# Optimization experiments

Measured on AMD Instinct MI355X. Metric: run time of the kernel, lower is better.

The kernel has to match this reference:

```python
import jax, jax.numpy as jnp
import numpy as np

B, HR, WR, C, HEADS, WS = 32, 64, 64, 128, 4, 8
HD = C // HEADS            # head dim = 32
N = WS * WS                # tokens per window = 64
NB = (2 * WS - 1) ** 2     # relative-bias table rows = 225
EPS = 1e-5


def _relative_bias_index():
    # Static int index, identical to SwinMSA._get_relative_bias_index
    coords = np.stack(np.meshgrid(np.arange(WS), np.arange(WS), indexing='ij'))  # (2, ws, ws)
    flat = coords.reshape(2, -1)                      # (2, n)
    rel = flat[:, :, None] - flat[:, None, :]         # (2, n, n)
    rel = rel.transpose(1, 2, 0).copy()               # (n, n, 2)
    rel[:, :, 0] += WS - 1
    rel[:, :, 1] += WS - 1
    rel[:, :, 0] *= 2 * WS - 1
    return rel.sum(-1)                                # (n, n) int

_REL_IDX = _relative_bias_index()


def _ln(x, g, b):
    m = jnp.mean(x, axis=-1, keepdims=True)
    v = jnp.mean(jnp.square(x - m), axis=-1, keepdims=True)
    return (x - m) * jax.lax.rsqrt(v + EPS) * g + b


def setup_inputs() -> dict:
    key = jax.random.key(0)
    ks = jax.random.split(key, 16)
    s = 0.02
    return {
        'x': jax.random.normal(ks[0], (B, HR * WR, C), jnp.float32),
        'qkv_w': jax.random.normal(ks[1], (C, 3 * C), jnp.float32) * s,
        'qkv_b': jnp.zeros((3 * C,), jnp.float32),
        'proj_w': jax.random.normal(ks[2], (C, C), jnp.float32) * s,
        'proj_b': jnp.zeros((C,), jnp.float32),
        'rel_bias_table': jax.random.normal(ks[3], (NB, HEADS), jnp.float32) * s,
        'ln1_g': jnp.ones((C,), jnp.float32),
        'ln1_b': jnp.zeros((C,), jnp.float32),
        'ln2_g': jnp.ones((C,), jnp.float32),
        'ln2_b': jnp.zeros((C,), jnp.float32),
        'mlp_w1': jax.random.normal(ks[4], (C, 4 * C), jnp.float32) * s,
        'mlp_b1': jnp.zeros((4 * C,), jnp.float32),
        'mlp_w2': jax.random.normal(ks[5], (4 * C, C), jnp.float32) * s,
        'mlp_b2': jnp.zeros((C,), jnp.float32),
    }


def reference(x, qkv_w, qkv_b, proj_w, proj_b, rel_bias_table,
              ln1_g, ln1_b, ln2_g, ln2_b, mlp_w1, mlp_b1, mlp_w2, mlp_b2):
    b = x.shape[0]
    hb, wb = HR // WS, WR // WS
    img = x.reshape(b, HR, WR, C)
    n1 = _ln(img, ln1_g, ln1_b)
    # window_partition: '(wy h) (wx w)' split puts window coord OUTER (strided windows),
    # faithful to the source rearrange.
    part = n1.reshape(b, WS, hb, WS, wb, C).transpose(0, 2, 4, 1, 3, 5)
    part = part.reshape(b * hb * wb, N, C)            # (Bw, n, c)
    qkv = part @ qkv_w + qkv_b                        # (Bw, n, 3c)
    # rearrange 'b n (h d c) -> d b n h c': channel factors as (head, 3, head_dim)
    qkv = qkv.reshape(-1, N, HEADS, 3, HD)
    q, k, v = qkv[..., 0, :], qkv[..., 1, :], qkv[..., 2, :]   # (Bw, n, h, hd)
    energy = jnp.einsum('bqhe,bkhe->bqhk', q, k) * (HD ** -0.5)
    bias = rel_bias_table[_REL_IDX.reshape(-1)].reshape(N, N, HEADS)
    bias = bias.transpose(2, 0, 1)                    # (h, n, n)
    energy = energy + bias.transpose(1, 0, 2)[None]   # broadcast as (q, h, k)
    attn = jax.nn.softmax(energy, axis=-1)
    out = jnp.einsum('bihv,bvhd->bihd', attn, v).reshape(-1, N, C)
    out = out @ proj_w + proj_b                       # (Bw, n, c)
    # window_reverse (inverse of the strided partition)
    rev = out.reshape(b, hb, wb, WS, WS, C).transpose(0, 3, 1, 4, 2, 5)
    rev = rev.reshape(b, HR * WR, C)
    msa = x + rev
    h2 = _ln(msa, ln2_g, ln2_b)
    mlp = jax.nn.gelu(h2 @ mlp_w1 + mlp_b1, approximate=False) @ mlp_w2 + mlp_b2
    return msa + mlp
```

## Files before the change

### kernel.cpp

```cpp
#include <hip/hip_runtime.h>
#include <hip/hip_bf16.h>

typedef __attribute__((ext_vector_type(4))) float f32x4;
typedef __attribute__((ext_vector_type(8))) short bf16x8;
typedef __attribute__((ext_vector_type(4))) short bf16x4;
typedef unsigned short u16;

__device__ __forceinline__ short fbf(float f){
  __hip_bfloat16 h = __float2bfloat16(f);
  return *reinterpret_cast<short*>(&h);
}
__device__ __forceinline__ float bf2f(short s){
  return __uint_as_float(((unsigned)(unsigned short)s) << 16);
}

#define LOG2E 1.4426950408889634f

__global__ void repack_kernel(const float* __restrict__ qkv_w, const float* __restrict__ proj_w,
                              const float* __restrict__ w1, const float* __restrict__ w2,
                              const float* __restrict__ tbl,
                              u16* __restrict__ rq, u16* __restrict__ rp,
                              u16* __restrict__ r1, u16* __restrict__ r2,
                              float* __restrict__ be){
  const int i = blockIdx.x * 256 + threadIdx.x;
  const int j = i & 7, lane = (i >> 3) & 63, f = i >> 9;
  const int kr = (lane >> 4) * 8 + j;
  const int c16 = lane & 15;
  if (i < 49152){ int nt = f % 24, kk = f / 24; rq[i] = (u16)fbf(qkv_w[(kk*32 + kr)*384 + nt*16 + c16]); }
  if (i < 16384){ int nt = f & 7,  kk = f >> 3; rp[i] = (u16)fbf(proj_w[(kk*32 + kr)*128 + nt*16 + c16]); }
  if (i < 65536){ int nt = f & 31, kk = f >> 5; r1[i] = (u16)fbf(w1[(kk*32 + kr)*512 + nt*16 + c16]); }
  if (i < 65536){ int nt = f & 7,  kk = f >> 3; r2[i] = (u16)fbf(w2[(kk*32 + kr)*128 + nt*16 + c16]); }
  if (i < 16384){
    int rg = i & 3, ln = (i >> 2) & 63, g = i >> 8;
    int nt = g & 3, mt = (g >> 2) & 3, h = g >> 4;
    int row = mt*16 + (ln >> 4)*4 + rg;
    int col = nt*16 + (ln & 15);
    int rel = ((col >> 3) - (row >> 3) + 7) * 15 + ((col & 7) - (row & 7) + 7);
    be[i] = tbl[rel*4 + h] * LOG2E;
  }
}

__global__ __launch_bounds__(256, 3)
void block_kernel(const float* __restrict__ x,
                  const float* __restrict__ qkv_b, const float* __restrict__ proj_b,
                  const float* __restrict__ ln1_g, const float* __restrict__ ln1_b,
                  const float* __restrict__ ln2_g, const float* __restrict__ ln2_b,
                  const u16* __restrict__ rep_qkv, const u16* __restrict__ rep_proj,
                  const u16* __restrict__ rep_w1, const u16* __restrict__ rep_w2,
                  const float* __restrict__ mlp_b1, const float* __restrict__ mlp_b2,
                  const float* __restrict__ bias_exp,
                  float* __restrict__ out){
  __shared__ __align__(16) u16 smem[24576];
  u16* sLN = smem;
  u16* sQ  = smem;
  u16* sK  = smem + 8192;
  u16* sV  = smem + 16384;
  u16* sP  = smem;
  u16* sO  = smem;
  u16* stg = smem + 8192;
  u16* sH  = smem + 16384;
  u16* sG  = smem;

  const int tid = threadIdx.x, lane = tid & 63, wid = tid >> 6;
  const int wdw = blockIdx.x;
  const int bb = wdw >> 6, ihb = (wdw >> 3) & 7, iwb = wdw & 7;
  const float* xb = x + (size_t)bb * 4096 * 128;
  float* ob = out + (size_t)bb * 4096 * 128;
  const f32x4 z4 = {0.f, 0.f, 0.f, 0.f};
  const int rb = tid >> 4, cb = tid & 15, c0g = cb * 8;
  const int r15 = lane & 15, kg = lane >> 4;

  {
    float g8[8], b8[8];
    *(f32x4*)&g8[0] = *(const f32x4*)(ln1_g + c0g);
    *(f32x4*)&g8[4] = *(const f32x4*)(ln1_g + c0g + 4);
    *(f32x4*)&b8[0] = *(const f32x4*)(ln1_b + c0g);
    *(f32x4*)&b8[4] = *(const f32x4*)(ln1_b + c0g + 4);
    #pragma unroll
    for (int it = 0; it < 4; ++it){
      const int r = it * 16 + rb;
      const int pix = ((r >> 3) * 8 + ihb) * 64 + (r & 7) * 8 + iwb;
      float fl[8];
      *(f32x4*)&fl[0] = *(const f32x4*)(xb + (size_t)pix * 128 + c0g);
      *(f32x4*)&fl[4] = *(const f32x4*)(xb + (size_t)pix * 128 + c0g + 4);
      float s = 0.f, sq = 0.f;
      #pragma unroll
      for (int j = 0; j < 8; ++j){ s += fl[j]; sq += fl[j]*fl[j]; }
      #pragma unroll
      for (int m = 1; m < 16; m <<= 1){ s += __shfl_xor(s, m); sq += __shfl_xor(sq, m); }
      const float mean = s * (1.f/128.f);
      const float rs = __builtin_amdgcn_rsqf(sq * (1.f/128.f) - mean*mean + 1e-5f);
      bf16x8 o;
      #pragma unroll
      for (int j = 0; j < 8; ++j) o[j] = fbf((fl[j]-mean)*rs*g8[j] + b8[j]);
      *(bf16x8*)&sLN[r*128 + (c0g ^ ((r & 7) << 3))] = o;
    }
  }
  __syncthreads();

  {
    f32x4 aqk[4][4];
    f32x4 av[4][2];
    #pragma unroll
    for (int ct = 0; ct < 4; ++ct){
      const f32x4 bq = *(const f32x4*)(qkv_b + wid*96 + ct*16 + kg*4);
      #pragma unroll
      for (int tt = 0; tt < 4; ++tt) aqk[ct][tt] = bq;
    }
    #pragma unroll
    for (int nt = 0; nt < 2; ++nt){
      const float bv = qkv_b[wid*96 + 64 + nt*16 + r15];
      const f32x4 bv4 = {bv, bv, bv, bv};
      #pragma unroll
      for (int mt = 0; mt < 4; ++mt) av[mt][nt] = bv4;
    }
    #pragma unroll
    for (int kk = 0; kk < 4; ++kk){
      bf16x8 L[4], aW[4], bWv[2];
      const int c0 = kk*32 + kg*8;
      #pragma unroll
      for (int t = 0; t < 4; ++t){
        const int row = t*16 + r15;
        L[t] = *(const bf16x8*)&sLN[row*128 + (c0 ^ ((row & 7) << 3))];
      }
      #pragma unroll
      for (int ct = 0; ct < 4; ++ct)
        aW[ct] = *(const bf16x8*)(rep_qkv + (size_t)((kk*24 + wid*6 + ct)*64 + lane)*8);
      #pragma unroll
      for (int nt = 0; nt < 2; ++nt)
        bWv[nt] = *(const bf16x8*)(rep_qkv + (size_t)((kk*24 + wid*6 + 4 + nt)*64 + lane)*8);
      #pragma unroll
      for (int ct = 0; ct < 4; ++ct)
        #pragma unroll
        for (int tt = 0; tt < 4; ++tt)
          aqk[ct][tt] = __builtin_amdgcn_mfma_f32_16x16x32_bf16(aW[ct], L[tt], aqk[ct][tt], 0, 0, 0);
      #pragma unroll
      for (int mt = 0; mt < 4; ++mt)
        #pragma unroll
        for (int nt = 0; nt < 2; ++nt)
          av[mt][nt] = __builtin_amdgcn_mfma_f32_16x16x32_bf16(L[mt], bWv[nt], av[mt][nt], 0, 0, 0);
    }
    __syncthreads();
    #pragma unroll
    for (int ct = 0; ct < 4; ++ct){
      u16* dst = (ct < 2) ? sQ : sK;
      const float scl = (ct < 2) ? 0.2550348296f : 1.0f;
      const int colu = wid*32 + (ct & 1)*16 + kg*4;
      #pragma unroll
      for (int tt = 0; tt < 4; ++tt){
        const int row = tt*16 + r15;
        bf16x4 pk;
        #pragma unroll
        for (int rg = 0; rg < 4; ++rg) pk[rg] = fbf(aqk[ct][tt][rg] * scl);
        *(bf16x4*)&dst[row*128 + (colu ^ ((row & 7) << 3))] = pk;
      }
    }
    #pragma unroll
    for (int nt = 0; nt < 2; ++nt){
      const int row = wid*32 + nt*16 + r15;
      #pragma unroll
      for (int mt = 0; mt < 4; ++mt){
        const int colu = mt*16 + kg*4;
        bf16x4 pk;
        #pragma unroll
        for (int rg = 0; rg < 4; ++rg) pk[rg] = fbf(av[mt][nt][rg]);
        *(bf16x4*)&sV[row*64 + (colu ^ ((row & 7) << 3))] = pk;
      }
    }
  }
  __syncthreads();

  f32x4 s4[4][4];
  {
    bf16x8 aK[4], bQ[4];
    #pragma unroll
    for (int t = 0; t < 4; ++t){
      const int row = t*16 + r15;
      const int off = (wid*32 + kg*8) ^ ((row & 7) << 3);
      aK[t] = *(const bf16x8*)&sK[row*128 + off];
      bQ[t] = *(const bf16x8*)&sQ[row*128 + off];
    }
    #pragma unroll
    for (int mtk = 0; mtk < 4; ++mtk)
      #pragma unroll
      for (int ntq = 0; ntq < 4; ++ntq){
        const f32x4 cb4 = *(const f32x4*)(bias_exp + (size_t)(((wid*4 + mtk)*4 + ntq)*64 + lane)*4);
        s4[mtk][ntq] = __builtin_amdgcn_mfma_f32_16x16x32_bf16(aK[mtk], bQ[ntq], cb4, 0, 0, 0);
      }
  }
  #pragma unroll
  for (int ntq = 0; ntq < 4; ++ntq){
    float sum = 0.f;
    #pragma unroll
    for (int mtk = 0; mtk < 4; ++mtk)
      #pragma unroll
      for (int rg = 0; rg < 4; ++rg){
        const float e = __builtin_amdgcn_exp2f(s4[mtk][ntq][rg]);
        s4[mtk][ntq][rg] = e; sum += e;
      }
    sum += __shfl_xor(sum, 16);
    sum += __shfl_xor(sum, 32);
    const float inv = __builtin_amdgcn_rcpf(sum);
    #pragma unroll
    for (int mtk = 0; mtk < 4; ++mtk)
      #pragma unroll
      for (int rg = 0; rg < 4; ++rg) s4[mtk][ntq][rg] *= inv;
  }
  __syncthreads();
  #pragma unroll
  for (int ntq = 0; ntq < 4; ++ntq){
    const int row = ntq*16 + r15;
    #pragma unroll
    for (int mtk = 0; mtk < 4; ++mtk){
      const int colu = mtk*16 + kg*4;
      bf16x4 pk;
      #pragma unroll
      for (int rg = 0; rg < 4; ++rg) pk[rg] = fbf(s4[mtk][ntq][rg]);
      *(bf16x4*)&sP[wid*4096 + row*64 + (colu ^ ((row & 7) << 3))] = pk;
    }
  }

  {
    f32x4 o4[2][4];
    #pragma unroll
    for (int dt = 0; dt < 2; ++dt)
      #pragma unroll
      for (int qt = 0; qt < 4; ++qt) o4[dt][qt] = z4;
    #pragma unroll
    for (int ks = 0; ks < 2; ++ks){
      bf16x8 aV[2], bP[4];
      #pragma unroll
      for (int dt = 0; dt < 2; ++dt){
        const int rowd = wid*32 + dt*16 + r15;
        aV[dt] = *(const bf16x8*)&sV[rowd*64 + ((ks*32 + kg*8) ^ ((rowd & 7) << 3))];
      }
      #pragma unroll
      for (int qt = 0; qt < 4; ++qt){
        const int rowq = qt*16 + r15;
        bP[qt] = *(const bf16x8*)&sP[wid*4096 + rowq*64 + ((ks*32 + kg*8) ^ ((rowq & 7) << 3))];
      }
      #pragma unroll
      for (int dt = 0; dt < 2; ++dt)
        #pragma unroll
        for (int qt = 0; qt < 4; ++qt)
          o4[dt][qt] = __builtin_amdgcn_mfma_f32_16x16x32_bf16(aV[dt], bP[qt], o4[dt][qt], 0, 0, 0);
    }
    __syncthreads();
    #pragma unroll
    for (int dt = 0; dt < 2; ++dt){
      const int dbase = wid*32 + dt*16 + kg*4;
      #pragma unroll
      for (int qt = 0; qt < 4; ++qt){
        const int q = qt*16 + r15;
        bf16x4 pk;
        #pragma unroll
        for (int rg = 0; rg < 4; ++rg) pk[rg] = fbf(o4[dt][qt][rg]);
        *(bf16x4*)&sO[q*128 + (dbase ^ ((q & 7) << 3))] = pk;
      }
    }
  }
  __syncthreads();

  {
    f32x4 xv[2][4];
    #pragma unroll
    for (int ot = 0; ot < 2; ++ot){
      const int cbase = (wid*2 + ot)*16 + kg*4;
      #pragma unroll
      for (int tt = 0; tt < 4; ++tt){
        const int tok = tt*16 + r15;
        const int pix = ((tok >> 3) * 8 + ihb) * 64 + (tok & 7) * 8 + iwb;
        xv[ot][tt] = *(const f32x4*)(xb + (size_t)pix * 128 + cbase);
      }
    }
    f32x4 po[2][4];
    #pragma unroll
    for (int ot = 0; ot < 2; ++ot){
      const f32x4 pb4 = *(const f32x4*)(proj_b + (wid*2 + ot)*16 + kg*4);
      #pragma unroll
      for (int tt = 0; tt < 4; ++tt) po[ot][tt] = pb4;
    }
    #pragma unroll
    for (int kk = 0; kk < 4; ++kk){
      bf16x8 aWp[2], bO[4];
      #pragma unroll
      for (int ot = 0; ot < 2; ++ot)
        aWp[ot] = *(const bf16x8*)(rep_proj + (size_t)((kk*8 + wid*2 + ot)*64 + lane)*8);
      #pragma unroll
      for (int tt = 0; tt < 4; ++tt){
        const int row = tt*16 + r15;
        bO[tt] = *(const bf16x8*)&sO[row*128 + ((kk*32 + kg*8) ^ ((row & 7) << 3))];
      }
      #pragma unroll
      for (int ot = 0; ot < 2; ++ot)
        #pragma unroll
        for (int tt = 0; tt < 4; ++tt)
          po[ot][tt] = __builtin_amdgcn_mfma_f32_16x16x32_bf16(aWp[ot], bO[tt], po[ot][tt], 0, 0, 0);
    }
    #pragma unroll
    for (int ot = 0; ot < 2; ++ot){
      const int cbase = (wid*2 + ot)*16 + kg*4;
      #pragma unroll
      for (int tt = 0; tt < 4; ++tt){
        const int tok = tt*16 + r15;
        bf16x4 pk;
        #pragma unroll
        for (int rg = 0; rg < 4; ++rg) pk[rg] = fbf(po[ot][tt][rg] + xv[ot][tt][rg]);
        *(bf16x4*)&stg[tok*128 + (cbase ^ ((tok & 7) << 3))] = pk;
      }
    }
  }
  __syncthreads();

  {
    float g8[8], b8[8];
    *(f32x4*)&g8[0] = *(const f32x4*)(ln2_g + c0g);
    *(f32x4*)&g8[4] = *(const f32x4*)(ln2_g + c0g + 4);
    *(f32x4*)&b8[0] = *(const f32x4*)(ln2_b + c0g);
    *(f32x4*)&b8[4] = *(const f32x4*)(ln2_b + c0g + 4);
    #pragma unroll
    for (int it = 0; it < 4; ++it){
      const int r = it * 16 + rb;
      bf16x8 m8 = *(const bf16x8*)&stg[r*128 + (c0g ^ ((r & 7) << 3))];
      float fl[8];
      #pragma unroll
      for (int j = 0; j < 8; ++j) fl[j] = bf2f(m8[j]);
      float s = 0.f, sq = 0.f;
      #pragma unroll
      for (int j = 0; j < 8; ++j){ s += fl[j]; sq += fl[j]*fl[j]; }
      #pragma unroll
      for (int m = 1; m < 16; m <<= 1){ s += __shfl_xor(s, m); sq += __shfl_xor(sq, m); }
      const float mean = s * (1.f/128.f);
      const float rs = __builtin_amdgcn_rsqf(sq * (1.f/128.f) - mean*mean + 1e-5f);
      bf16x8 o;
      #pragma unroll
      for (int j = 0; j < 8; ++j) o[j] = fbf((fl[j]-mean)*rs*g8[j] + b8[j]);
      *(bf16x8*)&sH[r*128 + (c0g ^ ((r & 7) << 3))] = o;
    }
  }
  __syncthreads();

  f32x4 accO[2][4];
  #pragma unroll
  for (int ot = 0; ot < 2; ++ot){
    const f32x4 b2v = *(const f32x4*)(mlp_b2 + (wid*2 + ot)*16 + kg*4);
    #pragma unroll
    for (int tt = 0; tt < 4; ++tt) accO[ot][tt] = b2v;
  }
  #pragma unroll
  for (int c = 0; c < 4; ++c){
    f32x4 t4[2][4];
    #pragma unroll
    for (int ht = 0; ht < 2; ++ht){
      const f32x4 b1v = *(const f32x4*)(mlp_b1 + c*128 + (wid*2 + ht)*16 + kg*4);
      #pragma unroll
      for (int tt = 0; tt < 4; ++tt) t4[ht][tt] = b1v;
    }
    #pragma unroll
    for (int kk = 0; kk < 4; ++kk){
      bf16x8 aW[2], bL[4];
      const int c0 = kk*32 + kg*8;
      #pragma unroll
      for (int ht = 0; ht < 2; ++ht)
        aW[ht] = *(const bf16x8*)(rep_w1 + (size_t)((kk*32 + c*8 + wid*2 + ht)*64 + lane)*8);
      #pragma unroll
      for (int tt = 0; tt < 4; ++tt){
        const int row = tt*16 + r15;
        bL[tt] = *(const bf16x8*)&sH[row*128 + (c0 ^ ((row & 7) << 3))];
      }
      #pragma unroll
      for (int ht = 0; ht < 2; ++ht)
        #pragma unroll
        for (int tt = 0; tt < 4; ++tt)
          t4[ht][tt] = __builtin_amdgcn_mfma_f32_16x16x32_bf16(aW[ht], bL[tt], t4[ht][tt], 0, 0, 0);
    }
    bf16x4 gp[2][4];
    #pragma unroll
    for (int ht = 0; ht < 2; ++ht)
      #pragma unroll
      for (int tt = 0; tt < 4; ++tt){
        #pragma unroll
        for (int rg = 0; rg < 4; ++rg){
          const float v = t4[ht][tt][rg];
          const float e = __builtin_amdgcn_exp2f(-2.4554669f * v);
          gp[ht][tt][rg] = fbf(v * __builtin_amdgcn_rcpf(1.f + e));
        }
      }
    __syncthreads();
    #pragma unroll
    for (int ht = 0; ht < 2; ++ht){
      const int colu = (wid*2 + ht)*16 + kg*4;
      #pragma unroll
      for (int tt = 0; tt < 4; ++tt){
        const int row = tt*16 + r15;
        *(bf16x4*)&sG[row*128 + (colu ^ ((row & 7) << 3))] = gp[ht][tt];
      }
    }
    __syncthreads();
    #pragma unroll
    for (int kk = 0; kk < 4; ++kk){
      bf16x8 aW2[2], bG[4];
      const int c0 = kk*32 + kg*8;
      #pragma unroll
      for (int ot = 0; ot < 2; ++ot)
        aW2[ot] = *(const bf16x8*)(rep_w2 + (size_t)(((c*4 + kk)*8 + wid*2 + ot)*64 + lane)*8);
      #pragma unroll
      for (int tt = 0; tt < 4; ++tt){
        const int row = tt*16 + r15;
        bG[tt] = *(const bf16x8*)&sG[row*128 + (c0 ^ ((row & 7) << 3))];
      }
      #pragma unroll
      for (int ot = 0; ot < 2; ++ot)
        #pragma unroll
        for (int tt = 0; tt < 4; ++tt)
          accO[ot][tt] = __builtin_amdgcn_mfma_f32_16x16x32_bf16(aW2[ot], bG[tt], accO[ot][tt], 0, 0, 0);
    }
  }

  #pragma unroll
  for (int ot = 0; ot < 2; ++ot){
    const int cbase = (wid*2 + ot)*16 + kg*4;
    #pragma unroll
    for (int tt = 0; tt < 4; ++tt){
      const int tok = tt*16 + r15;
      const int pix = ((tok >> 3) * 8 + ihb) * 64 + (tok & 7) * 8 + iwb;
      bf16x4 m4 = *(const bf16x4*)&stg[tok*128 + (cbase ^ ((tok & 7) << 3))];
      f32x4 o;
      #pragma unroll
      for (int rg = 0; rg < 4; ++rg) o[rg] = bf2f(m4[rg]) + accO[ot][tt][rg];
      *(f32x4*)(ob + (size_t)pix * 128 + cbase) = o;
    }
  }
}

extern "C" void kernel_launch(void* const* d_in, const int* in_sizes, int n_in,
                              void* d_out, int out_size, void* d_ws, size_t ws_size,
                              hipStream_t stream){
  (void)in_sizes; (void)n_in; (void)out_size; (void)ws_size;
  const float* x      = (const float*)d_in[0];
  const float* qkv_w  = (const float*)d_in[1];
  const float* qkv_b  = (const float*)d_in[2];
  const float* proj_w = (const float*)d_in[3];
  const float* proj_b = (const float*)d_in[4];
  const float* tbl    = (const float*)d_in[5];
  const float* ln1_g  = (const float*)d_in[6];
  const float* ln1_b  = (const float*)d_in[7];
  const float* ln2_g  = (const float*)d_in[8];
  const float* ln2_b  = (const float*)d_in[9];
  const float* w1     = (const float*)d_in[10];
  const float* b1     = (const float*)d_in[11];
  const float* w2     = (const float*)d_in[12];
  const float* b2     = (const float*)d_in[13];

  char* ws = (char*)d_ws;
  u16*   rq  = (u16*)ws;
  u16*   rp  = (u16*)(ws + 98304);
  u16*   r1  = (u16*)(ws + 131072);
  u16*   r2  = (u16*)(ws + 262144);
  float* be  = (float*)(ws + 393216);

  hipLaunchKernelGGL(repack_kernel, dim3(256), dim3(256), 0, stream,
                     qkv_w, proj_w, w1, w2, tbl, rq, rp, r1, r2, be);
  hipLaunchKernelGGL(block_kernel, dim3(2048), dim3(256), 0, stream,
                     x, qkv_b, proj_b, ln1_g, ln1_b, ln2_g, ln2_b,
                     rq, rp, r1, r2, b1, b2, be, (float*)d_out);
}
```

Measured before the change: 105.0 us.

## Shrink shared memory by storing V as fp8 e5m2 and halving MLP chunk width

Stores the V tile in shared memory as 8-bit e5m2 values, converted back to bf16 when loaded, and processes the MLP hidden dimension in 8 chunks of 64 instead of 4 chunks of 128. This lets sG shrink and the buffers overlap differently, cutting LDS per block from 48KB to 40KB so more blocks can be resident per CU. In exchange it adds conversion ALU work on V loads, loses precision on V (e5m2 has only 2 mantissa bits), and doubles the number of MLP chunk barriers.

```diff
diff --git a/kernel.cpp b/kernel.cpp
--- a/kernel.cpp
+++ b/kernel.cpp
@@ -1,10 +1,12 @@
 #include <hip/hip_runtime.h>
 #include <hip/hip_bf16.h>
+#include <hip/hip_fp16.h>
 
 typedef __attribute__((ext_vector_type(4))) float f32x4;
 typedef __attribute__((ext_vector_type(8))) short bf16x8;
 typedef __attribute__((ext_vector_type(4))) short bf16x4;
 typedef unsigned short u16;
+typedef unsigned char u8;
 
 __device__ __forceinline__ short fbf(float f){
   __hip_bfloat16 h = __float2bfloat16(f);
@@ -12,6 +14,17 @@
 }
 __device__ __forceinline__ float bf2f(short s){
   return __uint_as_float(((unsigned)(unsigned short)s) << 16);
+}
+__device__ __forceinline__ unsigned f2e5(float v){
+  __half h = __float2half(v);
+  unsigned hu = (unsigned)*reinterpret_cast<unsigned short*>(&h);
+  hu = hu + 0x7Fu + ((hu >> 8) & 1u);
+  return (hu >> 8) & 0xFFu;
+}
+__device__ __forceinline__ float e52f(unsigned b){
+  unsigned short hb = (unsigned short)(b << 8);
+  __half h = *reinterpret_cast<__half*>(&hb);
+  return __half2float(h);
 }
 
 #define LOG2E 1.4426950408889634f
@@ -50,16 +63,16 @@
                   const float* __restrict__ mlp_b1, const float* __restrict__ mlp_b2,
                   const float* __restrict__ bias_exp,
                   float* __restrict__ out){
-  __shared__ __align__(16) u16 smem[24576];
+  __shared__ __align__(16) u16 smem[20480];
   u16* sLN = smem;
   u16* sQ  = smem;
   u16* sK  = smem + 8192;
-  u16* sV  = smem + 16384;
   u16* sP  = smem;
   u16* sO  = smem;
   u16* stg = smem + 8192;
-  u16* sH  = smem + 16384;
-  u16* sG  = smem;
+  u16* sH  = smem;
+  u16* sG  = smem + 16384;
+  u8*  sVe5 = (u8*)(smem + 16384);
 
   const int tid = threadIdx.x, lane = tid & 63, wid = tid >> 6;
   const int wdw = blockIdx.x;
@@ -161,10 +174,9 @@
       #pragma unroll
       for (int mt = 0; mt < 4; ++mt){
         const int colu = mt*16 + kg*4;
-        bf16x4 pk;
-        #pragma unroll
-        for (int rg = 0; rg < 4; ++rg) pk[rg] = fbf(av[mt][nt][rg]);
-        *(bf16x4*)&sV[row*64 + (colu ^ ((row & 7) << 3))] = pk;
+        unsigned pk = f2e5(av[mt][nt][0]) | (f2e5(av[mt][nt][1]) << 8)
+                    | (f2e5(av[mt][nt][2]) << 16) | (f2e5(av[mt][nt][3]) << 24);
+        *(unsigned*)(sVe5 + row*64 + (colu ^ ((row & 7) << 3))) = pk;
       }
     }
   }
@@ -232,7 +244,16 @@
       #pragma unroll
       for (int dt = 0; dt < 2; ++dt){
         const int rowd = wid*32 + dt*16 + r15;
-        aV[dt] = *(const bf16x8*)&sV[rowd*64 + ((ks*32 + kg*8) ^ ((rowd & 7) << 3))];
+        const u8* pv = sVe5 + rowd*64 + ((ks*32 + kg*8) ^ ((rowd & 7) << 3));
+        const unsigned w0 = *(const unsigned*)pv;
+        const unsigned w1 = *(const unsigned*)(pv + 4);
+        bf16x8 a;
+        #pragma unroll
+        for (int j = 0; j < 4; ++j){
+          a[j]   = fbf(e52f((w0 >> (8*j)) & 0xFFu));
+          a[4+j] = fbf(e52f((w1 >> (8*j)) & 0xFFu));
+        }
+        aV[dt] = a;
       }
       #pragma unroll
       for (int qt = 0; qt < 4; ++qt){
@@ -348,66 +369,58 @@
     for (int tt = 0; tt < 4; ++tt) accO[ot][tt] = b2v;
   }
   #pragma unroll
-  for (int c = 0; c < 4; ++c){
-    f32x4 t4[2][4];
-    #pragma unroll
-    for (int ht = 0; ht < 2; ++ht){
-      const f32x4 b1v = *(const f32x4*)(mlp_b1 + c*128 + (wid*2 + ht)*16 + kg*4);
-      #pragma unroll
-      for (int tt = 0; tt < 4; ++tt) t4[ht][tt] = b1v;
+  for (int c = 0; c < 8; ++c){
+    f32x4 t4[4];
+    {
+      const f32x4 b1v = *(const f32x4*)(mlp_b1 + c*64 + wid*16 + kg*4);
+      #pragma unroll
+      for (int tt = 0; tt < 4; ++tt) t4[tt] = b1v;
     }
     #pragma unroll
     for (int kk = 0; kk < 4; ++kk){
-      bf16x8 aW[2], bL[4];
       const int c0 = kk*32 + kg*8;
-      #pragma unroll
-      for (int ht = 0; ht < 2; ++ht)
-        aW[ht] = *(const bf16x8*)(rep_w1 + (size_t)((kk*32 + c*8 + wid*2 + ht)*64 + lane)*8);
+      bf16x8 aW = *(const bf16x8*)(rep_w1 + (size_t)((kk*32 + c*4 + wid)*64 + lane)*8);
+      bf16x8 bL[4];
       #pragma unroll
       for (int tt = 0; tt < 4; ++tt){
         const int row = tt*16 + r15;
         bL[tt] = *(const bf16x8*)&sH[row*128 + (c0 ^ ((row & 7) << 3))];
       }
       #pragma unroll
-      for (int ht = 0; ht < 2; ++ht)
-        #pragma unroll
-        for (int tt = 0; tt < 4; ++tt)
-          t4[ht][tt] = __builtin_amdgcn_mfma_f32_16x16x32_bf16(aW[ht], bL[tt], t4[ht][tt], 0, 0, 0);
-    }
-    bf16x4 gp[2][4];
-    #pragma unroll
-    for (int ht = 0; ht < 2; ++ht)
-      #pragma unroll
-      for (int tt = 0; tt < 4; ++tt){
-        #pragma unroll
-        for (int rg = 0; rg < 4; ++rg){
-          const float v = t4[ht][tt][rg];
-          const float e = __builtin_amdgcn_exp2f(-2.4554669f * v);
-          gp[ht][tt][rg] = fbf(v * __builtin_amdgcn_rcpf(1.f + e));
-        }
-      }
+      for (int tt = 0; tt < 4; ++tt)
+        t4[tt] = __builtin_amdgcn_mfma_f32_16x16x32_bf16(aW, bL[tt], t4[tt], 0, 0, 0);
+    }
+    bf16x4 gp[4];
+    #pragma unroll
+    for (int tt = 0; tt < 4; ++tt){
+      #pragma unroll
+      for (int rg = 0; rg < 4; ++rg){
+        const float v = t4[tt][rg];
+        const float e = __builtin_amdgcn_exp2f(-2.4554669f * v);
+        gp[tt][rg] = fbf(v * __builtin_amdgcn_rcpf(1.f + e));
+      }
+    }
     __syncthreads();
-    #pragma unroll
-    for (int ht = 0; ht < 2; ++ht){
-      const int colu = (wid*2 + ht)*16 + kg*4;
+    {
+      const int colu = wid*16 + kg*4;
       #pragma unroll
       for (int tt = 0; tt < 4; ++tt){
         const int row = tt*16 + r15;
-        *(bf16x4*)&sG[row*128 + (colu ^ ((row & 7) << 3))] = gp[ht][tt];
+        *(bf16x4*)&sG[row*64 + (colu ^ ((row & 7) << 3))] = gp[tt];
       }
     }
     __syncthreads();
     #pragma unroll
-    for (int kk = 0; kk < 4; ++kk){
+    for (int kk2 = 0; kk2 < 2; ++kk2){
       bf16x8 aW2[2], bG[4];
-      const int c0 = kk*32 + kg*8;
+      const int c0 = kk2*32 + kg*8;
       #pragma unroll
       for (int ot = 0; ot < 2; ++ot)
-        aW2[ot] = *(const bf16x8*)(rep_w2 + (size_t)(((c*4 + kk)*8 + wid*2 + ot)*64 + lane)*8);
+        aW2[ot] = *(const bf16x8*)(rep_w2 + (size_t)(((c*2 + kk2)*8 + wid*2 + ot)*64 + lane)*8);
       #pragma unroll
       for (int tt = 0; tt < 4; ++tt){
         const int row = tt*16 + r15;
-        bG[tt] = *(const bf16x8*)&sG[row*128 + (c0 ^ ((row & 7) << 3))];
+        bG[tt] = *(const bf16x8*)&sG[row*64 + (c0 ^ ((row & 7) << 3))];
       }
       #pragma unroll
       for (int ot = 0; ot < 2; ++ot)
```

After: 103.9 us. Within noise of the previous version (-1.0%).
